# Kernel optimization log

Hardware: AMD Instinct MI355X
Metric: run time of the kernel (lower is better)

## Reference

```python
import jax, jax.numpy as jnp
import numpy as np

EPS = 1e-6

def _ln(x, w, b):
    m = x.mean(-1, keepdims=True)
    v = ((x - m) ** 2).mean(-1, keepdims=True)
    return (x - m) / jnp.sqrt(v + EPS) * w + b

def setup_inputs() -> dict:
    key = jax.random.key(0)
    ks = jax.random.split(key, 16)
    N, P, C, M = 8192, 64, 128, 4096
    MW = M * P  # 262144 gathered tokens
    A, BL = 131072, 65536
    x = jax.random.normal(ks[0], (N, P, C), dtype=jnp.float32)
    index_window = jax.random.permutation(ks[1], N)[:M]
    index_partition = jax.random.permutation(ks[2], MW)
    perm2 = jax.random.permutation(ks[3], MW)
    asy_index = perm2[:A]
    blocked_index = perm2[A:A + BL]
    p = lambda k, sh: 0.02 * jax.random.normal(k, sh, dtype=jnp.float32)
    return {
        "x": x,
        "index_window": index_window,
        "index_partition": index_partition,
        "asy_index": asy_index,
        "blocked_index": blocked_index,
        "M": M,
        "B": N,
        "ln1_w": jnp.ones((C,), jnp.float32), "ln1_b": jnp.zeros((C,), jnp.float32),
        "qkv_w": p(ks[4], (C, 3 * C)), "qkv_b": jnp.zeros((3 * C,), jnp.float32),
        "proj_w": p(ks[5], (C, C)), "proj_b": jnp.zeros((C,), jnp.float32),
        "gamma1": jnp.full((C,), 1e-1, jnp.float32),
        "ln2_w": jnp.ones((C,), jnp.float32), "ln2_b": jnp.zeros((C,), jnp.float32),
        "mlp_w1": p(ks[6], (C, 4 * C)), "mlp_b1": jnp.zeros((4 * C,), jnp.float32),
        "mlp_w2": p(ks[7], (4 * C, C)), "mlp_b2": jnp.zeros((C,), jnp.float32),
        "gamma2": jnp.full((C,), 1e-1, jnp.float32),
    }

def reference(x, index_window, index_partition, asy_index, blocked_index, M, B,
              ln1_w, ln1_b, qkv_w, qkv_b, proj_w, proj_b, gamma1,
              ln2_w, ln2_b, mlp_w1, mlp_b1, mlp_w2, mlp_b2, gamma2):
    N, P, C = x.shape
    H, dh = 4, 32
    scale = dh ** -0.5
    MW = index_partition.shape[0]
    x = _ln(x, ln1_w, ln1_b)                      # first_norm over whole input
    X = x                                          # (N, P, C)
    xw = x[index_window].reshape(-1, C)            # gather windows -> (MW, C)
    XX = xw
    xa = _ln(xw[asy_index], ln1_w, ln1_b)          # second norm on asy tokens
    xw = xw.at[asy_index].set(xa)
    shortcut = xa                                  # (A, C)
    xp = xw[index_partition].reshape(M, -1, C)     # (M, P, C) attention groups
    qkv = (xp @ qkv_w + qkv_b).reshape(M, P, H, 3 * dh).transpose(0, 2, 1, 3)
    q, k, v = jnp.split(qkv, 3, axis=3)            # each (M, H, P, dh)
    attn = jnp.einsum('mhqd,mhkd->mhqk', q, k) * scale
    # scatter scores keyed by key-token into flat map, mask blocked keys, gather back
    am = jnp.zeros((MW, P, H), attn.dtype)
    am = am.at[index_partition].set(jnp.transpose(attn, (0, 3, 2, 1)).reshape(MW, P, H))
    am = am.at[blocked_index].set(-10000.0)
    attn = jnp.transpose(am[index_partition].reshape(M, P, P, H), (0, 3, 2, 1))
    attn = jax.nn.softmax(attn, axis=-1)
    o = jnp.einsum('mhqk,mhkd->mhqd', attn, v).transpose(0, 2, 1, 3).reshape(M, P, C)
    o = o @ proj_w + proj_b
    XX = XX.at[index_partition].set(o.reshape(-1, C))
    y = XX[asy_index]
    # sub_layers: [ls1, droppath(id), ln2, mlp, ls2, droppath(id)]
    y = y * gamma1                                 # i=0
    y = shortcut + y                               # i=1 residual
    shortcut = y
    y2 = _ln(y, ln2_w, ln2_b)                      # i=2
    y2 = jax.nn.gelu(y2 @ mlp_w1 + mlp_b1, approximate=False) @ mlp_w2 + mlp_b2  # i=3
    y2 = y2 * gamma2                               # i=4
    y = shortcut + y2                              # i=5 residual
    XX = XX.at[asy_index].set(y)
    XX = XX.at[blocked_index].set(X[index_window].reshape(-1, C)[blocked_index])
    X = X.at[index_window].set(XX.reshape(M, -1, C))
    return X
```

## Files before the change

### kernel.cpp

```cpp
#include <hip/hip_runtime.h>
#include <hip/hip_bf16.h>
#include <math.h>

#define N_   8192
#define P_   64
#define C_   128
#define M_   4096
#define MW_  (M_ * P_)
#define A_   131072
#define BL_  65536
#define NROWS_ (N_ * P_)

typedef __attribute__((ext_vector_type(8))) __bf16 bf16x8;
typedef __attribute__((ext_vector_type(4))) float f32x4;
typedef __attribute__((ext_vector_type(2))) __bf16 bf16x2;

__device__ __forceinline__ float wave_sum(float v) {
#pragma unroll
  for (int o = 32; o > 0; o >>= 1) v += __shfl_xor(v, o, 64);
  return v;
}

__global__ __launch_bounds__(256) void k_set8(unsigned char* p, int n) {
  int i = blockIdx.x * 256 + threadIdx.x;
  if (i < n) p[i] = 0;
}
__global__ __launch_bounds__(256) void k_scatter2(unsigned char* p,
                                                  const int* __restrict__ ia,
                                                  const int* __restrict__ ib) {
  int i = blockIdx.x * 256 + threadIdx.x;
  if (i < A_) p[ia[i]] = 1;
  else {
    int j = i - A_;
    if (j < BL_) p[ib[j]] = 2;
  }
}

__global__ __launch_bounds__(256) void k_prep(const float* __restrict__ qkvw,
                                              const float* __restrict__ projw,
                                              const float* __restrict__ w1,
                                              const float* __restrict__ w2,
                                              __bf16* __restrict__ qkvt,
                                              __bf16* __restrict__ projt,
                                              __bf16* __restrict__ w1t,
                                              __bf16* __restrict__ w2t) {
  int i = blockIdx.x * 256 + threadIdx.x;
  if (i < 384 * 128) {
    int col = i >> 7, row = i & 127;
    qkvt[i] = (__bf16)qkvw[row * 384 + col];
  } else if (i < 384 * 128 + 128 * 128) {
    int j = i - 384 * 128;
    int col = j >> 7, row = j & 127;
    projt[j] = (__bf16)projw[row * 128 + col];
  } else if (i < 384 * 128 + 128 * 128 + 512 * 128) {
    int j = i - 384 * 128 - 128 * 128;
    int col = j >> 7, row = j & 127;
    w1t[j] = (__bf16)w1[row * 512 + col];
  } else {
    int j = i - 384 * 128 - 128 * 128 - 512 * 128;
    int col = j >> 9, row = j & 511;
    w2t[j] = (__bf16)w2[row * 128 + col];
  }
}

__global__ __launch_bounds__(256) void k_ln_all(const float* __restrict__ x,
                                                const float* __restrict__ w,
                                                const float* __restrict__ b,
                                                float* __restrict__ out) {
  int hw = threadIdx.x >> 5, l = threadIdx.x & 31;
  size_t row = (size_t)blockIdx.x * 8 + hw;
  float4 v = ((const float4*)(x + row * 128))[l];
  float s = (v.x + v.y) + (v.z + v.w);
#pragma unroll
  for (int o = 1; o < 32; o <<= 1) s += __shfl_xor(s, o, 64);
  float mean = s * (1.0f / 128.0f);
  float d0 = v.x - mean, d1 = v.y - mean, d2 = v.z - mean, d3 = v.w - mean;
  float q = (d0 * d0 + d1 * d1) + (d2 * d2 + d3 * d3);
#pragma unroll
  for (int o = 1; o < 32; o <<= 1) q += __shfl_xor(q, o, 64);
  float inv = rsqrtf(q * (1.0f / 128.0f) + 1e-6f);
  float4 wv = ((const float4*)w)[l];
  float4 bv = ((const float4*)b)[l];
  float4 o4;
  o4.x = d0 * inv * wv.x + bv.x;
  o4.y = d1 * inv * wv.y + bv.y;
  o4.z = d2 * inv * wv.z + bv.z;
  o4.w = d3 * inv * wv.w + bv.w;
  ((float4*)(out + row * 128))[l] = o4;
}

__global__ __launch_bounds__(256, 3) void k_attn(
    const int* __restrict__ iw,
    const int* __restrict__ ip, const unsigned char* __restrict__ flags,
    const float* __restrict__ ln1w, const float* __restrict__ ln1b,
    const __bf16* __restrict__ qkvt, const float* __restrict__ qkvb,
    const __bf16* __restrict__ projt, const float* __restrict__ projb,
    float* out) {
  __shared__ __align__(16) __bf16 XV[64 * 132];
  __shared__ __align__(16) __bf16 scratch[4 * 4352];
  __shared__ int srow[64];
  __shared__ unsigned char fl[64];

  const int tid = threadIdx.x;
  const int w = tid >> 6, lane = tid & 63;
  const int quad = lane >> 4, cl = lane & 15;
  const int m = blockIdx.x;

  if (tid < 64) {
    int s = ip[(m << 6) + tid];
    fl[tid] = flags[s];
    srow[tid] = iw[s >> 6] * 64 + (s & 63);
  }
  __syncthreads();

  __bf16* Xs = XV;
  const float lw0 = ln1w[2 * lane], lw1 = ln1w[2 * lane + 1];
  const float lb0 = ln1b[2 * lane], lb1 = ln1b[2 * lane + 1];

  {
    float2 xv[16];
#pragma unroll
    for (int ii = 0; ii < 16; ++ii) {
      int r = w + 4 * ii;
      xv[ii] = ((const float2*)(out + (size_t)srow[r] * 128))[lane];
    }
#pragma unroll
    for (int ii = 0; ii < 16; ++ii) {
      int r = w + 4 * ii;
      float y0 = xv[ii].x, y1 = xv[ii].y;
      if (fl[r] == 1) {
        float mean = wave_sum(y0 + y1) * (1.0f / 128.0f);
        float d0 = y0 - mean, d1 = y1 - mean;
        float inv = rsqrtf(wave_sum(d0 * d0 + d1 * d1) * (1.0f / 128.0f) + 1e-6f);
        y0 = d0 * inv * lw0 + lb0;
        y1 = d1 * inv * lw1 + lb1;
      }
      bf16x2 p2;
      p2[0] = (__bf16)y0; p2[1] = (__bf16)y1;
      *(bf16x2*)&Xs[r * 132 + 2 * lane] = p2;
    }
  }
  __syncthreads();

  __bf16* wsc = scratch + w * 4352;
  __bf16* Qs  = wsc;
  __bf16* Ks  = wsc + 2176;
  __bf16* Vts = XV + w * 2112;
  __bf16* Ps  = wsc;
  __bf16* Os  = wsc;
  const int h = w;

  bf16x8 af[4][4];
#pragma unroll
  for (int mt = 0; mt < 4; ++mt)
#pragma unroll
    for (int kt = 0; kt < 4; ++kt)
      af[mt][kt] = *(const bf16x8*)&Xs[(mt * 16 + cl) * 132 + kt * 32 + quad * 8];
  __syncthreads();

#pragma unroll
  for (int t = 0; t < 3; ++t) {
#pragma unroll
    for (int nt = 0; nt < 2; ++nt) {
      int col = h * 96 + t * 32 + nt * 16 + cl;
      bf16x8 bfr[4];
#pragma unroll
      for (int kt = 0; kt < 4; ++kt)
        bfr[kt] = *(const bf16x8*)&qkvt[(size_t)col * 128 + kt * 32 + quad * 8];
      float bias = qkvb[col];
      __builtin_amdgcn_s_setprio(1);
#pragma unroll
      for (int mt = 0; mt < 4; ++mt) {
        f32x4 acc = {bias, bias, bias, bias};
#pragma unroll
        for (int kt = 0; kt < 4; ++kt)
          acc = __builtin_amdgcn_mfma_f32_16x16x32_bf16(af[mt][kt], bfr[kt], acc, 0, 0, 0);
        if (t == 0) {
#pragma unroll
          for (int r = 0; r < 4; ++r)
            Qs[(mt * 16 + quad * 4 + r) * 34 + nt * 16 + cl] = (__bf16)acc[r];
        } else if (t == 1) {
#pragma unroll
          for (int r = 0; r < 4; ++r)
            Ks[(mt * 16 + quad * 4 + r) * 34 + nt * 16 + cl] = (__bf16)acc[r];
        } else {
#pragma unroll
          for (int r = 0; r < 4; ++r)
            Vts[(nt * 16 + cl) * 66 + mt * 16 + quad * 4 + r] = (__bf16)acc[r];
        }
      }
      __builtin_amdgcn_s_setprio(0);
    }
  }

  f32x4 sc4[4][4];
  {
    bf16x8 bk[4];
#pragma unroll
    for (int nt = 0; nt < 4; ++nt)
      bk[nt] = *(const bf16x8*)&Ks[(nt * 16 + cl) * 34 + quad * 8];
    __builtin_amdgcn_s_setprio(1);
#pragma unroll
    for (int mt = 0; mt < 4; ++mt) {
      bf16x8 aq = *(const bf16x8*)&Qs[(mt * 16 + cl) * 34 + quad * 8];
#pragma unroll
      for (int nt = 0; nt < 4; ++nt) {
        f32x4 z = {0.f, 0.f, 0.f, 0.f};
        sc4[mt][nt] = __builtin_amdgcn_mfma_f32_16x16x32_bf16(aq, bk[nt], z, 0, 0, 0);
      }
    }
    __builtin_amdgcn_s_setprio(0);
  }
  const float scale = 0.17677669529663687f;
  bool blk[4];
#pragma unroll
  for (int nt = 0; nt < 4; ++nt) blk[nt] = (fl[nt * 16 + cl] == 2);
#pragma unroll
  for (int mt = 0; mt < 4; ++mt)
#pragma unroll
    for (int nt = 0; nt < 4; ++nt)
#pragma unroll
      for (int r = 0; r < 4; ++r) {
        float v = sc4[mt][nt][r];
        sc4[mt][nt][r] = blk[nt] ? -10000.0f : v * scale;
      }
#pragma unroll
  for (int mt = 0; mt < 4; ++mt) {
#pragma unroll
    for (int r = 0; r < 4; ++r) {
      float mx = fmaxf(fmaxf(sc4[mt][0][r], sc4[mt][1][r]),
                       fmaxf(sc4[mt][2][r], sc4[mt][3][r]));
#pragma unroll
      for (int off = 1; off < 16; off <<= 1) mx = fmaxf(mx, __shfl_xor(mx, off, 64));
      float e0 = __expf(sc4[mt][0][r] - mx);
      float e1 = __expf(sc4[mt][1][r] - mx);
      float e2 = __expf(sc4[mt][2][r] - mx);
      float e3 = __expf(sc4[mt][3][r] - mx);
      float sm = (e0 + e1) + (e2 + e3);
#pragma unroll
      for (int off = 1; off < 16; off <<= 1) sm += __shfl_xor(sm, off, 64);
      float inv = 1.0f / sm;
      int row = mt * 16 + quad * 4 + r;
      Ps[row * 68 +  0 + cl] = (__bf16)(e0 * inv);
      Ps[row * 68 + 16 + cl] = (__bf16)(e1 * inv);
      Ps[row * 68 + 32 + cl] = (__bf16)(e2 * inv);
      Ps[row * 68 + 48 + cl] = (__bf16)(e3 * inv);
    }
  }

  f32x4 oacc[4][2];
  {
    bf16x8 bv[2][2];
#pragma unroll
    for (int nt = 0; nt < 2; ++nt)
#pragma unroll
      for (int kt = 0; kt < 2; ++kt)
        bv[nt][kt] = *(const bf16x8*)&Vts[(nt * 16 + cl) * 66 + kt * 32 + quad * 8];
    __builtin_amdgcn_s_setprio(1);
#pragma unroll
    for (int mt = 0; mt < 4; ++mt) {
      bf16x8 ap0 = *(const bf16x8*)&Ps[(mt * 16 + cl) * 68 + quad * 8];
      bf16x8 ap1 = *(const bf16x8*)&Ps[(mt * 16 + cl) * 68 + 32 + quad * 8];
#pragma unroll
      for (int nt = 0; nt < 2; ++nt) {
        f32x4 z = {0.f, 0.f, 0.f, 0.f};
        z = __builtin_amdgcn_mfma_f32_16x16x32_bf16(ap0, bv[nt][0], z, 0, 0, 0);
        z = __builtin_amdgcn_mfma_f32_16x16x32_bf16(ap1, bv[nt][1], z, 0, 0, 0);
        oacc[mt][nt] = z;
      }
    }
    __builtin_amdgcn_s_setprio(0);
  }
#pragma unroll
  for (int mt = 0; mt < 4; ++mt)
#pragma unroll
    for (int nt = 0; nt < 2; ++nt)
#pragma unroll
      for (int r = 0; r < 4; ++r)
        Os[(mt * 16 + quad * 4 + r) * 36 + nt * 16 + cl] = (__bf16)oacc[mt][nt][r];
  __syncthreads();

  const int jw = w * 32;
#pragma unroll
  for (int mt = 0; mt < 4; ++mt) {
#pragma unroll
    for (int nt = 0; nt < 2; ++nt) {
      int col = jw + nt * 16 + cl;
      float pb = projb[col];
      f32x4 acc = {pb, pb, pb, pb};
#pragma unroll
      for (int kt = 0; kt < 4; ++kt) {
        const __bf16* op = scratch + kt * 4352;
        bf16x8 a = *(const bf16x8*)&op[(mt * 16 + cl) * 36 + quad * 8];
        bf16x8 bb = *(const bf16x8*)&projt[(size_t)col * 128 + kt * 32 + quad * 8];
        acc = __builtin_amdgcn_mfma_f32_16x16x32_bf16(a, bb, acc, 0, 0, 0);
      }
#pragma unroll
      for (int r = 0; r < 4; ++r) {
        int row = mt * 16 + quad * 4 + r;
        if (fl[row] != 2)
          out[(size_t)srow[row] * 128 + col] = acc[r];
      }
    }
  }
}

__global__ __launch_bounds__(256, 5) void k_mlp(
    const float* __restrict__ x, const int* __restrict__ iw,
    const int* __restrict__ ia,
    const float* __restrict__ ln1w, const float* __restrict__ ln1b,
    const float* __restrict__ g1,
    const float* __restrict__ ln2w, const float* __restrict__ ln2b,
    const __bf16* __restrict__ w1t, const float* __restrict__ b1,
    const __bf16* __restrict__ w2t, const float* __restrict__ b2,
    const float* __restrict__ g2,
    float* out) {
  __shared__ __align__(16) __bf16 y2s[64 * 136];
  __shared__ __align__(16) __bf16 hb[64 * 68];
  __shared__ int wrs[64];

  const int tid = threadIdx.x;
  const int w = tid >> 6, lane = tid & 63;
  const int quad = lane >> 4, cl = lane & 15;

  if (tid < 64) {
    int s = ia[(blockIdx.x << 6) + tid];
    wrs[tid] = iw[s >> 6] * 64 + (s & 63);
  }
  __syncthreads();

  const float lw0 = ln1w[2 * lane], lw1 = ln1w[2 * lane + 1];
  const float lb0 = ln1b[2 * lane], lb1 = ln1b[2 * lane + 1];
  const float g1a = g1[2 * lane], g1b = g1[2 * lane + 1];
  const float l2w0 = ln2w[2 * lane], l2w1 = ln2w[2 * lane + 1];
  const float l2b0 = ln2b[2 * lane], l2b1 = ln2b[2 * lane + 1];

  for (int q4 = 0; q4 < 4; ++q4) {
    float2 xv[4], ov[4];
#pragma unroll
    for (int ii = 0; ii < 4; ++ii) {
      int r = w + 4 * (q4 * 4 + ii);
      size_t wr = (size_t)wrs[r];
      xv[ii] = ((const float2*)(x + wr * 128))[lane];
      ov[ii] = ((const float2*)(out + wr * 128))[lane];
    }
#pragma unroll
    for (int ii = 0; ii < 4; ++ii) {
      int r = w + 4 * (q4 * 4 + ii);
      float mean = wave_sum(xv[ii].x + xv[ii].y) * (1.0f / 128.0f);
      float d0 = xv[ii].x - mean, d1 = xv[ii].y - mean;
      float inv = rsqrtf(wave_sum(d0 * d0 + d1 * d1) * (1.0f / 128.0f) + 1e-6f);
      float y0 = d0 * inv * lw0 + lb0, y1 = d1 * inv * lw1 + lb1;
      mean = wave_sum(y0 + y1) * (1.0f / 128.0f);
      d0 = y0 - mean; d1 = y1 - mean;
      inv = rsqrtf(wave_sum(d0 * d0 + d1 * d1) * (1.0f / 128.0f) + 1e-6f);
      float xa0 = d0 * inv * lw0 + lb0, xa1 = d1 * inv * lw1 + lb1;
      float yv0 = xa0 + g1a * ov[ii].x;
      float yv1 = xa1 + g1b * ov[ii].y;
      ((float2*)(out + (size_t)wrs[r] * 128))[lane] = make_float2(yv0, yv1);
      mean = wave_sum(yv0 + yv1) * (1.0f / 128.0f);
      d0 = yv0 - mean; d1 = yv1 - mean;
      inv = rsqrtf(wave_sum(d0 * d0 + d1 * d1) * (1.0f / 128.0f) + 1e-6f);
      bf16x2 p2;
      p2[0] = (__bf16)(d0 * inv * l2w0 + l2b0);
      p2[1] = (__bf16)(d1 * inv * l2w1 + l2b1);
      *(bf16x2*)&y2s[r * 136 + 2 * lane] = p2;
    }
  }
  __threadfence_block();
  __syncthreads();

  f32x4 zacc[4][2];
#pragma unroll
  for (int nt = 0; nt < 2; ++nt) {
    float bb = b2[w * 32 + nt * 16 + cl];
#pragma unroll
    for (int mt = 0; mt < 4; ++mt) zacc[mt][nt] = (f32x4){bb, bb, bb, bb};
  }

  for (int ch = 0; ch < 8; ++ch) {
    {
      int col = ch * 64 + w * 16 + cl;
      bf16x8 bfr[4];
#pragma unroll
      for (int kt = 0; kt < 4; ++kt)
        bfr[kt] = *(const bf16x8*)&w1t[(size_t)col * 128 + kt * 32 + quad * 8];
      float bias = b1[col];
      __builtin_amdgcn_s_setprio(1);
#pragma unroll
      for (int mt = 0; mt < 4; ++mt) {
        f32x4 acc = {bias, bias, bias, bias};
#pragma unroll
        for (int kt = 0; kt < 4; ++kt) {
          bf16x8 a = *(const bf16x8*)&y2s[(mt * 16 + cl) * 136 + kt * 32 + quad * 8];
          acc = __builtin_amdgcn_mfma_f32_16x16x32_bf16(a, bfr[kt], acc, 0, 0, 0);
        }
#pragma unroll
        for (int r = 0; r < 4; ++r) {
          float a = acc[r];
          float g = a * 0.5f * (1.0f + erff(a * 0.70710678118654752f));
          hb[(mt * 16 + quad * 4 + r) * 68 + w * 16 + cl] = (__bf16)g;
        }
      }
      __builtin_amdgcn_s_setprio(0);
    }
    __syncthreads();
#pragma unroll
    for (int nt = 0; nt < 2; ++nt) {
      int col = w * 32 + nt * 16 + cl;
      bf16x8 bfr[2];
#pragma unroll
      for (int kk = 0; kk < 2; ++kk)
        bfr[kk] = *(const bf16x8*)&w2t[(size_t)col * 512 + ch * 64 + kk * 32 + quad * 8];
      __builtin_amdgcn_s_setprio(1);
#pragma unroll
      for (int mt = 0; mt < 4; ++mt)
#pragma unroll
        for (int kk = 0; kk < 2; ++kk) {
          bf16x8 a = *(const bf16x8*)&hb[(mt * 16 + cl) * 68 + kk * 32 + quad * 8];
          zacc[mt][nt] = __builtin_amdgcn_mfma_f32_16x16x32_bf16(a, bfr[kk],
                                                                zacc[mt][nt], 0, 0, 0);
        }
      __builtin_amdgcn_s_setprio(0);
    }
    __syncthreads();
  }

#pragma unroll
  for (int mt = 0; mt < 4; ++mt)
#pragma unroll
    for (int nt = 0; nt < 2; ++nt) {
      int col = w * 32 + nt * 16 + cl;
      float gg = g2[col];
#pragma unroll
      for (int r = 0; r < 4; ++r) {
        int row = mt * 16 + quad * 4 + r;
        size_t a = (size_t)wrs[row] * 128 + col;
        out[a] = out[a] + gg * zacc[mt][nt][r];
      }
    }
}

extern "C" void kernel_launch(void* const* d_in, const int* in_sizes, int n_in,
                              void* d_out, int out_size, void* d_ws, size_t ws_size,
                              hipStream_t stream) {
  const float* x = (const float*)d_in[0];
  const int* iw = (const int*)d_in[1];
  const int* ip = (const int*)d_in[2];
  const int* ia = (const int*)d_in[3];
  const int* ib = (const int*)d_in[4];
  const float* ln1w = (const float*)d_in[7];
  const float* ln1b = (const float*)d_in[8];
  const float* qkvw = (const float*)d_in[9];
  const float* qkvb = (const float*)d_in[10];
  const float* projw = (const float*)d_in[11];
  const float* projb = (const float*)d_in[12];
  const float* g1 = (const float*)d_in[13];
  const float* ln2w = (const float*)d_in[14];
  const float* ln2b = (const float*)d_in[15];
  const float* w1 = (const float*)d_in[16];
  const float* b1 = (const float*)d_in[17];
  const float* w2 = (const float*)d_in[18];
  const float* b2 = (const float*)d_in[19];
  const float* g2 = (const float*)d_in[20];
  float* out = (float*)d_out;

  unsigned char* flags = (unsigned char*)d_ws;
  __bf16* qkvt = (__bf16*)((char*)d_ws + MW_);
  __bf16* projt = (__bf16*)((char*)d_ws + MW_ + 384 * 128 * 2);
  __bf16* w1t = (__bf16*)((char*)d_ws + MW_ + 384 * 128 * 2 + 128 * 128 * 2);
  __bf16* w2t = (__bf16*)((char*)d_ws + MW_ + 384 * 128 * 2 + 128 * 128 * 2 + 512 * 128 * 2);

  k_set8<<<MW_ / 256, 256, 0, stream>>>(flags, MW_);
  k_scatter2<<<(A_ + BL_) / 256, 256, 0, stream>>>(flags, ia, ib);
  k_prep<<<(384 * 128 + 128 * 128 + 512 * 128 + 128 * 512) / 256, 256, 0, stream>>>(
      qkvw, projw, w1, w2, qkvt, projt, w1t, w2t);
  k_ln_all<<<NROWS_ / 8, 256, 0, stream>>>(x, ln1w, ln1b, out);
  k_attn<<<M_, 256, 0, stream>>>(iw, ip, flags, ln1w, ln1b, qkvt, qkvb,
                                 projt, projb, out);
  k_mlp<<<A_ / 64, 256, 0, stream>>>(x, iw, ia, ln1w, ln1b, g1, ln2w, ln2b,
                                     w1t, b1, w2t, b2, g2, out);
}
```

Before: 803.5 us.

## Fuse residual, LN2 and MLP into attention kernel, dropping separate MLP pass

Removes the separate k_mlp launch and performs the gamma1 residual, LN2, MLP and gamma2 residual inside k_attn for asy-flagged rows. The saved LN statistics from the second norm are reused, so x no longer has to be re-read and LN1 is not recomputed twice, and the intermediate out round trip is avoided. Projection weights are also hoisted out of the mt loop. The cost is that every attention block now runs the full MLP over all 64 rows, including non-asy rows (about half). It also adds more register and shared memory pressure under the 3-blocks-per-CU launch bound.

After: 956.4 us. 1.19x slower.

```diff
diff --git a/kernel.cpp b/kernel.cpp
--- a/kernel.cpp
+++ b/kernel.cpp
@@ -95,11 +95,18 @@
     const float* __restrict__ ln1w, const float* __restrict__ ln1b,
     const __bf16* __restrict__ qkvt, const float* __restrict__ qkvb,
     const __bf16* __restrict__ projt, const float* __restrict__ projb,
+    const float* __restrict__ g1,
+    const float* __restrict__ ln2w, const float* __restrict__ ln2b,
+    const __bf16* __restrict__ w1t, const float* __restrict__ b1,
+    const __bf16* __restrict__ w2t, const float* __restrict__ b2,
+    const float* __restrict__ g2,
     float* out) {
   __shared__ __align__(16) __bf16 XV[64 * 132];
   __shared__ __align__(16) __bf16 scratch[4 * 4352];
   __shared__ int srow[64];
   __shared__ unsigned char fl[64];
+  __shared__ float sm2[64];
+  __shared__ float si2[64];
 
   const int tid = threadIdx.x;
   const int w = tid >> 6, lane = tid & 63;
@@ -132,6 +139,7 @@
         float mean = wave_sum(y0 + y1) * (1.0f / 128.0f);
         float d0 = y0 - mean, d1 = y1 - mean;
         float inv = rsqrtf(wave_sum(d0 * d0 + d1 * d1) * (1.0f / 128.0f) + 1e-6f);
+        if (lane == 0) { sm2[r] = mean; si2[r] = inv; }
         y0 = d0 * inv * lw0 + lb0;
         y1 = d1 * inv * lw1 + lb1;
       }
@@ -271,6 +279,7 @@
     }
     __builtin_amdgcn_s_setprio(0);
   }
+  __syncthreads();
 #pragma unroll
   for (int mt = 0; mt < 4; ++mt)
 #pragma unroll
@@ -281,120 +290,125 @@
   __syncthreads();
 
   const int jw = w * 32;
-#pragma unroll
-  for (int mt = 0; mt < 4; ++mt) {
-#pragma unroll
-    for (int nt = 0; nt < 2; ++nt) {
-      int col = jw + nt * 16 + cl;
-      float pb = projb[col];
+  f32x4 op4[4][2];
+#pragma unroll
+  for (int nt = 0; nt < 2; ++nt) {
+    int col = jw + nt * 16 + cl;
+    float pb = projb[col];
+    bf16x8 bpr[4];
+#pragma unroll
+    for (int kt = 0; kt < 4; ++kt)
+      bpr[kt] = *(const bf16x8*)&projt[(size_t)col * 128 + kt * 32 + quad * 8];
+#pragma unroll
+    for (int mt = 0; mt < 4; ++mt) {
       f32x4 acc = {pb, pb, pb, pb};
 #pragma unroll
       for (int kt = 0; kt < 4; ++kt) {
         const __bf16* op = scratch + kt * 4352;
         bf16x8 a = *(const bf16x8*)&op[(mt * 16 + cl) * 36 + quad * 8];
-        bf16x8 bb = *(const bf16x8*)&projt[(size_t)col * 128 + kt * 32 + quad * 8];
-        acc = __builtin_amdgcn_mfma_f32_16x16x32_bf16(a, bb, acc, 0, 0, 0);
-      }
+        acc = __builtin_amdgcn_mfma_f32_16x16x32_bf16(a, bpr[kt], acc, 0, 0, 0);
+      }
+      op4[mt][nt] = acc;
 #pragma unroll
       for (int r = 0; r < 4; ++r) {
         int row = mt * 16 + quad * 4 + r;
-        if (fl[row] != 2)
+        if (fl[row] == 0)
           out[(size_t)srow[row] * 128 + col] = acc[r];
       }
     }
   }
-}
-
-__global__ __launch_bounds__(256, 5) void k_mlp(
-    const float* __restrict__ x, const int* __restrict__ iw,
-    const int* __restrict__ ia,
-    const float* __restrict__ ln1w, const float* __restrict__ ln1b,
-    const float* __restrict__ g1,
-    const float* __restrict__ ln2w, const float* __restrict__ ln2b,
-    const __bf16* __restrict__ w1t, const float* __restrict__ b1,
-    const __bf16* __restrict__ w2t, const float* __restrict__ b2,
-    const float* __restrict__ g2,
-    float* out) {
-  __shared__ __align__(16) __bf16 y2s[64 * 136];
-  __shared__ __align__(16) __bf16 hb[64 * 68];
-  __shared__ int wrs[64];
-
-  const int tid = threadIdx.x;
-  const int w = tid >> 6, lane = tid & 63;
-  const int quad = lane >> 4, cl = lane & 15;
-
-  if (tid < 64) {
-    int s = ia[(blockIdx.x << 6) + tid];
-    wrs[tid] = iw[s >> 6] * 64 + (s & 63);
-  }
-  __syncthreads();
-
-  const float lw0 = ln1w[2 * lane], lw1 = ln1w[2 * lane + 1];
-  const float lb0 = ln1b[2 * lane], lb1 = ln1b[2 * lane + 1];
-  const float g1a = g1[2 * lane], g1b = g1[2 * lane + 1];
-  const float l2w0 = ln2w[2 * lane], l2w1 = ln2w[2 * lane + 1];
-  const float l2b0 = ln2b[2 * lane], l2b1 = ln2b[2 * lane + 1];
-
-  for (int q4 = 0; q4 < 4; ++q4) {
-    float2 xv[4], ov[4];
-#pragma unroll
-    for (int ii = 0; ii < 4; ++ii) {
-      int r = w + 4 * (q4 * 4 + ii);
-      size_t wr = (size_t)wrs[r];
-      xv[ii] = ((const float2*)(x + wr * 128))[lane];
-      ov[ii] = ((const float2*)(out + wr * 128))[lane];
-    }
-#pragma unroll
-    for (int ii = 0; ii < 4; ++ii) {
-      int r = w + 4 * (q4 * 4 + ii);
-      float mean = wave_sum(xv[ii].x + xv[ii].y) * (1.0f / 128.0f);
-      float d0 = xv[ii].x - mean, d1 = xv[ii].y - mean;
-      float inv = rsqrtf(wave_sum(d0 * d0 + d1 * d1) * (1.0f / 128.0f) + 1e-6f);
-      float y0 = d0 * inv * lw0 + lb0, y1 = d1 * inv * lw1 + lb1;
-      mean = wave_sum(y0 + y1) * (1.0f / 128.0f);
-      d0 = y0 - mean; d1 = y1 - mean;
-      inv = rsqrtf(wave_sum(d0 * d0 + d1 * d1) * (1.0f / 128.0f) + 1e-6f);
-      float xa0 = d0 * inv * lw0 + lb0, xa1 = d1 * inv * lw1 + lb1;
-      float yv0 = xa0 + g1a * ov[ii].x;
-      float yv1 = xa1 + g1b * ov[ii].y;
-      ((float2*)(out + (size_t)wrs[r] * 128))[lane] = make_float2(yv0, yv1);
-      mean = wave_sum(yv0 + yv1) * (1.0f / 128.0f);
-      d0 = yv0 - mean; d1 = yv1 - mean;
-      inv = rsqrtf(wave_sum(d0 * d0 + d1 * d1) * (1.0f / 128.0f) + 1e-6f);
-      bf16x2 p2;
-      p2[0] = (__bf16)(d0 * inv * l2w0 + l2b0);
-      p2[1] = (__bf16)(d1 * inv * l2w1 + l2b1);
-      *(bf16x2*)&y2s[r * 136 + 2 * lane] = p2;
-    }
-  }
-  __threadfence_block();
-  __syncthreads();
+  __syncthreads();
+
+  float* yf = (float*)scratch;
+  __bf16* hb = XV;
+
+  float g1c[2], lwc[2], lbc[2], g2c[2], b2c[2];
+#pragma unroll
+  for (int nt = 0; nt < 2; ++nt) {
+    int col = jw + nt * 16 + cl;
+    g1c[nt] = g1[col]; lwc[nt] = ln1w[col]; lbc[nt] = ln1b[col];
+    g2c[nt] = g2[col]; b2c[nt] = b2[col];
+  }
+
+#pragma unroll
+  for (int mt = 0; mt < 4; ++mt)
+#pragma unroll
+    for (int nt = 0; nt < 2; ++nt) {
+      int col = jw + nt * 16 + cl;
+#pragma unroll
+      for (int r = 0; r < 4; ++r) {
+        int row = mt * 16 + quad * 4 + r;
+        float v = 0.f;
+        if (fl[row] == 1) {
+          float lnv = out[(size_t)srow[row] * 128 + col];
+          float xa = (lnv - sm2[row]) * si2[row] * lwc[nt] + lbc[nt];
+          v = xa + g1c[nt] * op4[mt][nt][r];
+        }
+        yf[row * 132 + col] = v;
+      }
+    }
+  __syncthreads();
+
+#pragma unroll
+  for (int ii = 0; ii < 16; ++ii) {
+    int r = w + 4 * ii;
+    float a0 = yf[r * 132 + 2 * lane];
+    float a1 = yf[r * 132 + 2 * lane + 1];
+    float mean = wave_sum(a0 + a1) * (1.0f / 128.0f);
+    float d0 = a0 - mean, d1 = a1 - mean;
+    float inv = rsqrtf(wave_sum(d0 * d0 + d1 * d1) * (1.0f / 128.0f) + 1e-6f);
+    if (lane == 0) { sm2[r] = mean; si2[r] = inv; }
+  }
+  __syncthreads();
+
+  bf16x8 afy[4][4];
+#pragma unroll
+  for (int kt = 0; kt < 4; ++kt) {
+    float4 wva = ((const float4*)(ln2w + kt * 32 + quad * 8))[0];
+    float4 wvb = ((const float4*)(ln2w + kt * 32 + quad * 8))[1];
+    float4 bva = ((const float4*)(ln2b + kt * 32 + quad * 8))[0];
+    float4 bvb = ((const float4*)(ln2b + kt * 32 + quad * 8))[1];
+#pragma unroll
+    for (int mt = 0; mt < 4; ++mt) {
+      int row = mt * 16 + cl;
+      float mm = sm2[row], iv = si2[row];
+      f32x4 va = *(const f32x4*)&yf[row * 132 + kt * 32 + quad * 8];
+      f32x4 vb = *(const f32x4*)&yf[row * 132 + kt * 32 + quad * 8 + 4];
+      bf16x8 o8;
+      o8[0] = (__bf16)((va[0] - mm) * iv * wva.x + bva.x);
+      o8[1] = (__bf16)((va[1] - mm) * iv * wva.y + bva.y);
+      o8[2] = (__bf16)((va[2] - mm) * iv * wva.z + bva.z);
+      o8[3] = (__bf16)((va[3] - mm) * iv * wva.w + bva.w);
+      o8[4] = (__bf16)((vb[0] - mm) * iv * wvb.x + bvb.x);
+      o8[5] = (__bf16)((vb[1] - mm) * iv * wvb.y + bvb.y);
+      o8[6] = (__bf16)((vb[2] - mm) * iv * wvb.z + bvb.z);
+      o8[7] = (__bf16)((vb[3] - mm) * iv * wvb.w + bvb.w);
+      afy[mt][kt] = o8;
+    }
+  }
 
   f32x4 zacc[4][2];
 #pragma unroll
-  for (int nt = 0; nt < 2; ++nt) {
-    float bb = b2[w * 32 + nt * 16 + cl];
-#pragma unroll
-    for (int mt = 0; mt < 4; ++mt) zacc[mt][nt] = (f32x4){bb, bb, bb, bb};
-  }
+  for (int nt = 0; nt < 2; ++nt)
+#pragma unroll
+    for (int mt = 0; mt < 4; ++mt)
+      zacc[mt][nt] = (f32x4){b2c[nt], b2c[nt], b2c[nt], b2c[nt]};
 
   for (int ch = 0; ch < 8; ++ch) {
     {
-      int col = ch * 64 + w * 16 + cl;
-      bf16x8 bfr[4];
+      int col1 = ch * 64 + w * 16 + cl;
+      bf16x8 b1f[4];
 #pragma unroll
       for (int kt = 0; kt < 4; ++kt)
-        bfr[kt] = *(const bf16x8*)&w1t[(size_t)col * 128 + kt * 32 + quad * 8];
-      float bias = b1[col];
+        b1f[kt] = *(const bf16x8*)&w1t[(size_t)col1 * 128 + kt * 32 + quad * 8];
+      float bias1 = b1[col1];
       __builtin_amdgcn_s_setprio(1);
 #pragma unroll
       for (int mt = 0; mt < 4; ++mt) {
-        f32x4 acc = {bias, bias, bias, bias};
-#pragma unroll
-        for (int kt = 0; kt < 4; ++kt) {
-          bf16x8 a = *(const bf16x8*)&y2s[(mt * 16 + cl) * 136 + kt * 32 + quad * 8];
-          acc = __builtin_amdgcn_mfma_f32_16x16x32_bf16(a, bfr[kt], acc, 0, 0, 0);
-        }
+        f32x4 acc = {bias1, bias1, bias1, bias1};
+#pragma unroll
+        for (int kt = 0; kt < 4; ++kt)
+          acc = __builtin_amdgcn_mfma_f32_16x16x32_bf16(afy[mt][kt], b1f[kt], acc, 0, 0, 0);
 #pragma unroll
         for (int r = 0; r < 4; ++r) {
           float a = acc[r];
@@ -407,19 +421,19 @@
     __syncthreads();
 #pragma unroll
     for (int nt = 0; nt < 2; ++nt) {
-      int col = w * 32 + nt * 16 + cl;
-      bf16x8 bfr[2];
+      int colz = jw + nt * 16 + cl;
+      bf16x8 b2f[2];
 #pragma unroll
       for (int kk = 0; kk < 2; ++kk)
-        bfr[kk] = *(const bf16x8*)&w2t[(size_t)col * 512 + ch * 64 + kk * 32 + quad * 8];
+        b2f[kk] = *(const bf16x8*)&w2t[(size_t)colz * 512 + ch * 64 + kk * 32 + quad * 8];
       __builtin_amdgcn_s_setprio(1);
 #pragma unroll
       for (int mt = 0; mt < 4; ++mt)
 #pragma unroll
         for (int kk = 0; kk < 2; ++kk) {
           bf16x8 a = *(const bf16x8*)&hb[(mt * 16 + cl) * 68 + kk * 32 + quad * 8];
-          zacc[mt][nt] = __builtin_amdgcn_mfma_f32_16x16x32_bf16(a, bfr[kk],
-                                                                zacc[mt][nt], 0, 0, 0);
+          zacc[mt][nt] = __builtin_amdgcn_mfma_f32_16x16x32_bf16(a, b2f[kk],
+                                                                 zacc[mt][nt], 0, 0, 0);
         }
       __builtin_amdgcn_s_setprio(0);
     }
@@ -430,13 +444,13 @@
   for (int mt = 0; mt < 4; ++mt)
 #pragma unroll
     for (int nt = 0; nt < 2; ++nt) {
-      int col = w * 32 + nt * 16 + cl;
-      float gg = g2[col];
+      int col = jw + nt * 16 + cl;
 #pragma unroll
       for (int r = 0; r < 4; ++r) {
         int row = mt * 16 + quad * 4 + r;
-        size_t a = (size_t)wrs[row] * 128 + col;
-        out[a] = out[a] + gg * zacc[mt][nt][r];
+        if (fl[row] == 1)
+          out[(size_t)srow[row] * 128 + col] =
+              yf[row * 132 + col] + g2c[nt] * zacc[mt][nt][r];
       }
     }
 }
@@ -477,7 +491,6 @@
       qkvw, projw, w1, w2, qkvt, projt, w1t, w2t);
   k_ln_all<<<NROWS_ / 8, 256, 0, stream>>>(x, ln1w, ln1b, out);
   k_attn<<<M_, 256, 0, stream>>>(iw, ip, flags, ln1w, ln1b, qkvt, qkvb,
-                                 projt, projb, out);
-  k_mlp<<<A_ / 64, 256, 0, stream>>>(x, iw, ia, ln1w, ln1b, g1, ln2w, ln2b,
-                                     w1t, b1, w2t, b2, g2, out);
-}
+                                 projt, projb, g1, ln2w, ln2b,
+                                 w1t, b1, w2t, b2, g2, out);
+}
```

## Fuse LN/prep/flag-clear kernels and double MLP rows per block

Applied to the files above, without the earlier changes.

Merges the flag-zeroing, weight transpose/convert and first-layernorm kernels into one launch to cut launch count and serialization. The MLP kernel now processes 128 tokens per block instead of 64, so each weight fragment loaded from global memory is reused across twice as many rows. This doubles the shared-memory footprint and the accumulator registers, and the occupancy hint drops from 5 to 3 blocks, which may reduce latency hiding.

After: 836.2 us. 4.1% more time.

```diff
diff --git a/kernel.cpp b/kernel.cpp
--- a/kernel.cpp
+++ b/kernel.cpp
@@ -10,6 +10,9 @@
 #define A_   131072
 #define BL_  65536
 #define NROWS_ (N_ * P_)
+#define LNBLK_   (NROWS_ / 8)
+#define PREPBLK_ (196608 / 256)
+#define SETBLK_  (MW_ / 256)
 
 typedef __attribute__((ext_vector_type(8))) __bf16 bf16x8;
 typedef __attribute__((ext_vector_type(4))) float f32x4;
@@ -21,10 +24,6 @@
   return v;
 }
 
-__global__ __launch_bounds__(256) void k_set8(unsigned char* p, int n) {
-  int i = blockIdx.x * 256 + threadIdx.x;
-  if (i < n) p[i] = 0;
-}
 __global__ __launch_bounds__(256) void k_scatter2(unsigned char* p,
                                                   const int* __restrict__ ia,
                                                   const int* __restrict__ ib) {
@@ -36,37 +35,41 @@
   }
 }
 
-__global__ __launch_bounds__(256) void k_prep(const float* __restrict__ qkvw,
-                                              const float* __restrict__ projw,
-                                              const float* __restrict__ w1,
-                                              const float* __restrict__ w2,
-                                              __bf16* __restrict__ qkvt,
-                                              __bf16* __restrict__ projt,
-                                              __bf16* __restrict__ w1t,
-                                              __bf16* __restrict__ w2t) {
-  int i = blockIdx.x * 256 + threadIdx.x;
-  if (i < 384 * 128) {
-    int col = i >> 7, row = i & 127;
-    qkvt[i] = (__bf16)qkvw[row * 384 + col];
-  } else if (i < 384 * 128 + 128 * 128) {
-    int j = i - 384 * 128;
-    int col = j >> 7, row = j & 127;
-    projt[j] = (__bf16)projw[row * 128 + col];
-  } else if (i < 384 * 128 + 128 * 128 + 512 * 128) {
-    int j = i - 384 * 128 - 128 * 128;
-    int col = j >> 7, row = j & 127;
-    w1t[j] = (__bf16)w1[row * 512 + col];
-  } else {
-    int j = i - 384 * 128 - 128 * 128 - 512 * 128;
-    int col = j >> 9, row = j & 511;
-    w2t[j] = (__bf16)w2[row * 128 + col];
-  }
-}
-
-__global__ __launch_bounds__(256) void k_ln_all(const float* __restrict__ x,
-                                                const float* __restrict__ w,
-                                                const float* __restrict__ b,
-                                                float* __restrict__ out) {
+__global__ __launch_bounds__(256) void k_ln_prep_set(
+    const float* __restrict__ x,
+    const float* __restrict__ w, const float* __restrict__ b,
+    const float* __restrict__ qkvw, const float* __restrict__ projw,
+    const float* __restrict__ w1, const float* __restrict__ w2,
+    __bf16* __restrict__ qkvt, __bf16* __restrict__ projt,
+    __bf16* __restrict__ w1t, __bf16* __restrict__ w2t,
+    unsigned char* __restrict__ flags,
+    float* __restrict__ out) {
+  if (blockIdx.x >= LNBLK_) {
+    int bx = blockIdx.x - LNBLK_;
+    if (bx >= PREPBLK_) {
+      int i = (bx - PREPBLK_) * 256 + threadIdx.x;
+      flags[i] = 0;
+      return;
+    }
+    int i = bx * 256 + threadIdx.x;
+    if (i < 384 * 128) {
+      int col = i >> 7, row = i & 127;
+      qkvt[i] = (__bf16)qkvw[row * 384 + col];
+    } else if (i < 384 * 128 + 128 * 128) {
+      int j = i - 384 * 128;
+      int col = j >> 7, row = j & 127;
+      projt[j] = (__bf16)projw[row * 128 + col];
+    } else if (i < 384 * 128 + 128 * 128 + 512 * 128) {
+      int j = i - 384 * 128 - 128 * 128;
+      int col = j >> 7, row = j & 127;
+      w1t[j] = (__bf16)w1[row * 512 + col];
+    } else {
+      int j = i - 384 * 128 - 128 * 128 - 512 * 128;
+      int col = j >> 9, row = j & 511;
+      w2t[j] = (__bf16)w2[row * 128 + col];
+    }
+    return;
+  }
   int hw = threadIdx.x >> 5, l = threadIdx.x & 31;
   size_t row = (size_t)blockIdx.x * 8 + hw;
   float4 v = ((const float4*)(x + row * 128))[l];
@@ -305,7 +308,7 @@
   }
 }
 
-__global__ __launch_bounds__(256, 5) void k_mlp(
+__global__ __launch_bounds__(256, 3) void k_mlp(
     const float* __restrict__ x, const int* __restrict__ iw,
     const int* __restrict__ ia,
     const float* __restrict__ ln1w, const float* __restrict__ ln1b,
@@ -315,16 +318,16 @@
     const __bf16* __restrict__ w2t, const float* __restrict__ b2,
     const float* __restrict__ g2,
     float* out) {
-  __shared__ __align__(16) __bf16 y2s[64 * 136];
-  __shared__ __align__(16) __bf16 hb[64 * 68];
-  __shared__ int wrs[64];
+  __shared__ __align__(16) __bf16 y2s[128 * 136];
+  __shared__ __align__(16) __bf16 hb[128 * 68];
+  __shared__ int wrs[128];
 
   const int tid = threadIdx.x;
   const int w = tid >> 6, lane = tid & 63;
   const int quad = lane >> 4, cl = lane & 15;
 
-  if (tid < 64) {
-    int s = ia[(blockIdx.x << 6) + tid];
+  if (tid < 128) {
+    int s = ia[(blockIdx.x << 7) + tid];
     wrs[tid] = iw[s >> 6] * 64 + (s & 63);
   }
   __syncthreads();
@@ -335,18 +338,18 @@
   const float l2w0 = ln2w[2 * lane], l2w1 = ln2w[2 * lane + 1];
   const float l2b0 = ln2b[2 * lane], l2b1 = ln2b[2 * lane + 1];
 
-  for (int q4 = 0; q4 < 4; ++q4) {
+  for (int q = 0; q < 8; ++q) {
     float2 xv[4], ov[4];
 #pragma unroll
     for (int ii = 0; ii < 4; ++ii) {
-      int r = w + 4 * (q4 * 4 + ii);
+      int r = w + 4 * (q * 4 + ii);
       size_t wr = (size_t)wrs[r];
       xv[ii] = ((const float2*)(x + wr * 128))[lane];
       ov[ii] = ((const float2*)(out + wr * 128))[lane];
     }
 #pragma unroll
     for (int ii = 0; ii < 4; ++ii) {
-      int r = w + 4 * (q4 * 4 + ii);
+      int r = w + 4 * (q * 4 + ii);
       float mean = wave_sum(xv[ii].x + xv[ii].y) * (1.0f / 128.0f);
       float d0 = xv[ii].x - mean, d1 = xv[ii].y - mean;
       float inv = rsqrtf(wave_sum(d0 * d0 + d1 * d1) * (1.0f / 128.0f) + 1e-6f);
@@ -370,12 +373,12 @@
   __threadfence_block();
   __syncthreads();
 
-  f32x4 zacc[4][2];
+  f32x4 zacc[8][2];
 #pragma unroll
   for (int nt = 0; nt < 2; ++nt) {
     float bb = b2[w * 32 + nt * 16 + cl];
 #pragma unroll
-    for (int mt = 0; mt < 4; ++mt) zacc[mt][nt] = (f32x4){bb, bb, bb, bb};
+    for (int mt = 0; mt < 8; ++mt) zacc[mt][nt] = (f32x4){bb, bb, bb, bb};
   }
 
   for (int ch = 0; ch < 8; ++ch) {
@@ -388,7 +391,7 @@
       float bias = b1[col];
       __builtin_amdgcn_s_setprio(1);
 #pragma unroll
-      for (int mt = 0; mt < 4; ++mt) {
+      for (int mt = 0; mt < 8; ++mt) {
         f32x4 acc = {bias, bias, bias, bias};
 #pragma unroll
         for (int kt = 0; kt < 4; ++kt) {
@@ -414,7 +417,7 @@
         bfr[kk] = *(const bf16x8*)&w2t[(size_t)col * 512 + ch * 64 + kk * 32 + quad * 8];
       __builtin_amdgcn_s_setprio(1);
 #pragma unroll
-      for (int mt = 0; mt < 4; ++mt)
+      for (int mt = 0; mt < 8; ++mt)
 #pragma unroll
         for (int kk = 0; kk < 2; ++kk) {
           bf16x8 a = *(const bf16x8*)&hb[(mt * 16 + cl) * 68 + kk * 32 + quad * 8];
@@ -427,7 +430,7 @@
   }
 
 #pragma unroll
-  for (int mt = 0; mt < 4; ++mt)
+  for (int mt = 0; mt < 8; ++mt)
 #pragma unroll
     for (int nt = 0; nt < 2; ++nt) {
       int col = w * 32 + nt * 16 + cl;
@@ -471,13 +474,11 @@
   __bf16* w1t = (__bf16*)((char*)d_ws + MW_ + 384 * 128 * 2 + 128 * 128 * 2);
   __bf16* w2t = (__bf16*)((char*)d_ws + MW_ + 384 * 128 * 2 + 128 * 128 * 2 + 512 * 128 * 2);
 
-  k_set8<<<MW_ / 256, 256, 0, stream>>>(flags, MW_);
+  k_ln_prep_set<<<LNBLK_ + PREPBLK_ + SETBLK_, 256, 0, stream>>>(
+      x, ln1w, ln1b, qkvw, projw, w1, w2, qkvt, projt, w1t, w2t, flags, out);
   k_scatter2<<<(A_ + BL_) / 256, 256, 0, stream>>>(flags, ia, ib);
-  k_prep<<<(384 * 128 + 128 * 128 + 512 * 128 + 128 * 512) / 256, 256, 0, stream>>>(
-      qkvw, projw, w1, w2, qkvt, projt, w1t, w2t);
-  k_ln_all<<<NROWS_ / 8, 256, 0, stream>>>(x, ln1w, ln1b, out);
   k_attn<<<M_, 256, 0, stream>>>(iw, ip, flags, ln1w, ln1b, qkvt, qkvb,
                                  projt, projb, out);
-  k_mlp<<<A_ / 64, 256, 0, stream>>>(x, iw, ia, ln1w, ln1b, g1, ln2w, ln2b,
-                                     w1t, b1, w2t, b2, g2, out);
-}
+  k_mlp<<<A_ / 128, 256, 0, stream>>>(x, iw, ia, ln1w, ln1b, g1, ln2w, ln2b,
+                                      w1t, b1, w2t, b2, g2, out);
+}
```
